# Performance work log

Measured on AMD Instinct MI355X. Metric: run time of the kernel, lower is better.

Reference implementation:

```python
import jax, jax.numpy as jnp
import numpy as np

def setup_inputs() -> dict:
    key = jax.random.key(0)
    k1, k2, k3 = jax.random.split(key, 3)
    B, NC, NQ, D = 16, 1024, 128, 512
    c_vector = jax.random.normal(k1, (B, NC, D), dtype=jnp.float32)
    q_vector = jax.random.normal(k2, (B, NQ, D), dtype=jnp.float32)
    kernel = jax.random.normal(k3, (3 * D, 1), dtype=jnp.float32) * 0.05
    bias = jnp.ones((), dtype=jnp.float32)
    return {"c_vector": c_vector, "q_vector": q_vector, "kernel": kernel, "bias": bias}

def reference(c_vector, q_vector, kernel, bias):
    # sim[b,i,j] = w . [c_i ; q_j ; c_i*q_j] + bias, decomposed to avoid the
    # (B, n_c, n_q, 3d) intermediate of the original tile+concat formulation.
    D = c_vector.shape[-1]
    w = kernel[:, 0]                      # (3d,)
    w_c, w_q, w_cq = w[:D], w[D:2 * D], w[2 * D:]
    c_term = c_vector @ w_c               # (B, n_c)
    q_term = q_vector @ w_q               # (B, n_q)
    cq_term = jnp.einsum('bid,bjd->bij', c_vector * w_cq, q_vector)  # (B, n_c, n_q)
    return cq_term + c_term[:, :, None] + q_term[:, None, :] + bias
```

## Files before the change

### kernel.cpp

```cpp
#include <hip/hip_runtime.h>
#include <hip/hip_bf16.h>

#define B_   16
#define NC_  1024
#define NQ_  128
#define D_   512
#define NKT  8

typedef __attribute__((ext_vector_type(8))) short bf16x8;
typedef __attribute__((ext_vector_type(4))) float f32x4;

__device__ __forceinline__ short f2bf(float x) {
    return __builtin_bit_cast(short, __float2bfloat16(x));
}
__device__ __forceinline__ float bf2f(short s) {
    unsigned u = ((unsigned)(unsigned short)s) << 16;
    return __builtin_bit_cast(float, u);
}

__global__ __launch_bounds__(256, 2) void sim_kernel(
    const float* __restrict__ c, const float* __restrict__ q,
    const float* __restrict__ kern, const float* __restrict__ bias_p,
    float* __restrict__ out)
{
    __shared__ __align__(16) char  lds[2][16384];
    __shared__ __align__(16) short wl[1536];
    __shared__ __align__(16) float ctl[64];
    __shared__ __align__(16) float qtl[64];

    const int bid   = blockIdx.x;
    const int b     = ((bid & 7) << 1) | (bid >> 8);
    const int inner = (bid >> 3) & 31;
    const int mt    = inner >> 1;
    const int nb    = inner & 1;
    const int tid   = threadIdx.x;
    const int lane  = tid & 63;
    const int w     = tid >> 6;
    const int wm    = w >> 1, wn = w & 1;
    const int rif   = lane & 15;
    const int kg    = lane >> 4;

    if (tid < 192) {
        const float* s = kern + tid * 8;
        f32x4 v0 = *(const f32x4*)s;
        f32x4 v1 = *(const f32x4*)(s + 4);
        bf16x8 o;
        o[0]=f2bf(v0[0]); o[1]=f2bf(v0[1]); o[2]=f2bf(v0[2]); o[3]=f2bf(v0[3]);
        o[4]=f2bf(v1[0]); o[5]=f2bf(v1[1]); o[6]=f2bf(v1[2]); o[7]=f2bf(v1[3]);
        *(bf16x8*)&wl[tid * 8] = o;
    }

    const int ar0 = tid >> 3, ar1 = ar0 + 32;
    const int acs = (tid & 7) * 8;
    const float* ag0 = c + (size_t)(b * NC_ + mt * 64 + ar0) * D_ + acs;
    const float* ag1 = c + (size_t)(b * NC_ + mt * 64 + ar1) * D_ + acs;
    const int aw0 = ar0 * 128 + ((acs * 2)       ^ ((ar0 & 7) << 4));
    const int aw1 = ar1 * 128 + ((acs * 2)       ^ ((ar1 & 7) << 4));

    const int bj = tid >> 2, bp = tid & 3;
    const float* bg = q + (size_t)(b * NQ_ + nb * 64 + bj) * D_ + bp * 16;
    const int bw0 = 8192 + bj * 128 + ((bp * 32)      ^ ((bj & 7) << 4));
    const int bw1 = 8192 + bj * 128 + ((bp * 32 + 16) ^ ((bj & 7) << 4));

    f32x4 sa[2][4], sb[2][4];
    float ct0 = 0.f, ct1 = 0.f, qta = 0.f;
    f32x4 acc00 = {}, acc01 = {}, acc10 = {}, acc11 = {};

#define ISSUE(T)                                                   \
    do { const int s_ = (T) & 1;                                   \
        sa[s_][0] = *(const f32x4*)(ag0 + (T) * 64);               \
        sa[s_][1] = *(const f32x4*)(ag0 + (T) * 64 + 4);           \
        sa[s_][2] = *(const f32x4*)(ag1 + (T) * 64);               \
        sa[s_][3] = *(const f32x4*)(ag1 + (T) * 64 + 4);           \
        sb[s_][0] = *(const f32x4*)(bg + (T) * 64);                \
        sb[s_][1] = *(const f32x4*)(bg + (T) * 64 + 4);            \
        sb[s_][2] = *(const f32x4*)(bg + (T) * 64 + 8);            \
        sb[s_][3] = *(const f32x4*)(bg + (T) * 64 + 12);           \
    } while (0)

#define WRITE(T)                                                               \
    do { const int s_ = (T) & 1; char* Lw = &lds[s_][0];                       \
        bf16x8 wcq = *(const bf16x8*)&wl[1024 + (T) * 64 + acs];               \
        bf16x8 wc8 = *(const bf16x8*)&wl[       (T) * 64 + acs];               \
        bf16x8 wq0 = *(const bf16x8*)&wl[512  + (T) * 64 + bp * 16];           \
        bf16x8 wq1 = *(const bf16x8*)&wl[512  + (T) * 64 + bp * 16 + 8];       \
        bf16x8 oa0, oa1, ob0, ob1;                                             \
        _Pragma("unroll")                                                      \
        for (int e = 0; e < 8; ++e) {                                          \
            float wcqf = bf2f(wcq[e]);                                         \
            float x0 = sa[s_][e >> 2][e & 3];                                  \
            float x1 = sa[s_][2 + (e >> 2)][e & 3];                            \
            oa0[e] = f2bf(x0 * wcqf);                                          \
            oa1[e] = f2bf(x1 * wcqf);                                          \
            float wcf = bf2f(wc8[e]);                                          \
            ct0 += x0 * wcf;  ct1 += x1 * wcf;                                 \
            float y0 = sb[s_][e >> 2][e & 3];                                  \
            float y1 = sb[s_][2 + (e >> 2)][e & 3];                            \
            ob0[e] = f2bf(y0); ob1[e] = f2bf(y1);                              \
            qta += y0 * bf2f(wq0[e]) + y1 * bf2f(wq1[e]);                      \
        }                                                                      \
        *(bf16x8*)(Lw + aw0) = oa0;                                            \
        *(bf16x8*)(Lw + aw1) = oa1;                                            \
        *(bf16x8*)(Lw + bw0) = ob0;                                            \
        *(bf16x8*)(Lw + bw1) = ob1;                                            \
    } while (0)

#define COMPUTE(T)                                                                                   \
    do { const char* L = &lds[(T) & 1][0];                                                           \
        _Pragma("unroll")                                                                            \
        for (int kk = 0; kk < 2; ++kk) {                                                             \
            const int ks = kk * 64 + kg * 16;                                                        \
            bf16x8 af0, af1, bf0, bf1;                                                               \
            { int r = wm*32 + rif;      af0 = *(const bf16x8*)(L + r*128 + (ks ^ ((r & 7) << 4))); } \
            { int r = wm*32 + 16 + rif; af1 = *(const bf16x8*)(L + r*128 + (ks ^ ((r & 7) << 4))); } \
            { int j = wn*32 + rif;      bf0 = *(const bf16x8*)(L + 8192 + j*128 + (ks ^ ((j & 7) << 4))); } \
            { int j = wn*32 + 16 + rif; bf1 = *(const bf16x8*)(L + 8192 + j*128 + (ks ^ ((j & 7) << 4))); } \
            acc00 = __builtin_amdgcn_mfma_f32_16x16x32_bf16(af0, bf0, acc00, 0, 0, 0);               \
            acc01 = __builtin_amdgcn_mfma_f32_16x16x32_bf16(af0, bf1, acc01, 0, 0, 0);               \
            acc10 = __builtin_amdgcn_mfma_f32_16x16x32_bf16(af1, bf0, acc10, 0, 0, 0);               \
            acc11 = __builtin_amdgcn_mfma_f32_16x16x32_bf16(af1, bf1, acc11, 0, 0, 0);               \
        }                                                                                            \
    } while (0)

    ISSUE(0); ISSUE(1);
    asm volatile("s_waitcnt lgkmcnt(0)" ::: "memory");
    __builtin_amdgcn_sched_barrier(0);
    __builtin_amdgcn_s_barrier();
    WRITE(0);
    asm volatile("s_waitcnt lgkmcnt(0)" ::: "memory");
    __builtin_amdgcn_sched_barrier(0);
    __builtin_amdgcn_s_barrier();

    #pragma unroll
    for (int kt = 0; kt < NKT; ++kt) {
        if (kt + 2 < NKT) ISSUE(kt + 2);
        __builtin_amdgcn_sched_barrier(0);
        COMPUTE(kt);
        if (kt + 1 < NKT) {
            WRITE(kt + 1);
            asm volatile("s_waitcnt lgkmcnt(0)" ::: "memory");
            __builtin_amdgcn_sched_barrier(0);
            __builtin_amdgcn_s_barrier();
        }
    }
#undef ISSUE
#undef WRITE
#undef COMPUTE

    ct0 += __shfl_xor(ct0, 1); ct0 += __shfl_xor(ct0, 2); ct0 += __shfl_xor(ct0, 4);
    ct1 += __shfl_xor(ct1, 1); ct1 += __shfl_xor(ct1, 2); ct1 += __shfl_xor(ct1, 4);
    qta += __shfl_xor(qta, 1); qta += __shfl_xor(qta, 2);
    if ((tid & 7) == 0) { ctl[ar0] = ct0; ctl[ar1] = ct1; }
    if ((tid & 3) == 0) qtl[bj] = qta;
    asm volatile("s_waitcnt lgkmcnt(0)" ::: "memory");
    __builtin_amdgcn_sched_barrier(0);
    __builtin_amdgcn_s_barrier();

    const float bias = *bias_p;
    const int jc = wn * 32;
    const float qt0 = qtl[jc + rif]      + bias;
    const float qt1 = qtl[jc + 16 + rif] + bias;
    #pragma unroll
    for (int mf = 0; mf < 2; ++mf) {
        f32x4 ctv = *(const f32x4*)&ctl[wm * 32 + mf * 16 + kg * 4];
        float* o = out + ((size_t)(b * NC_ + mt * 64 + wm * 32 + mf * 16 + kg * 4)) * NQ_
                 + nb * 64 + jc + rif;
        const f32x4 a0 = mf ? acc10 : acc00;
        const f32x4 a1 = mf ? acc11 : acc01;
        #pragma unroll
        for (int r = 0; r < 4; ++r) {
            o[(size_t)r * NQ_ +  0] = a0[r] + ctv[r] + qt0;
            o[(size_t)r * NQ_ + 16] = a1[r] + ctv[r] + qt1;
        }
    }
}

extern "C" void kernel_launch(void* const* d_in, const int* in_sizes, int n_in,
                              void* d_out, int out_size, void* d_ws, size_t ws_size,
                              hipStream_t stream) {
    const float* c    = (const float*)d_in[0];
    const float* q    = (const float*)d_in[1];
    const float* kern = (const float*)d_in[2];
    const float* bias = (const float*)d_in[3];
    float* out = (float*)d_out;

    sim_kernel<<<512, 256, 0, stream>>>(c, q, kern, bias, out);
}
```

Measured before the change: 16.36 us.

## Double the K-tile to 128, move w_cq scaling onto Q, cut pipeline depth

```diff
diff --git a/kernel.cpp b/kernel.cpp
--- a/kernel.cpp
+++ b/kernel.cpp
@@ -5,7 +5,7 @@
 #define NC_  1024
 #define NQ_  128
 #define D_   512
-#define NKT  8
+#define NKT  4
 
 typedef __attribute__((ext_vector_type(8))) short bf16x8;
 typedef __attribute__((ext_vector_type(4))) float f32x4;
@@ -23,8 +23,10 @@
     const float* __restrict__ kern, const float* __restrict__ bias_p,
     float* __restrict__ out)
 {
-    __shared__ __align__(16) char  lds[2][16384];
-    __shared__ __align__(16) short wl[1536];
+    __shared__ __align__(16) char  lds[2][32768];
+    __shared__ __align__(16) short wcb[512];
+    __shared__ __align__(16) short wqb[512];
+    __shared__ __align__(16) short wcqb[512];
     __shared__ __align__(16) float ctl[64];
     __shared__ __align__(16) float qtl[64];
 
@@ -47,74 +49,68 @@
         bf16x8 o;
         o[0]=f2bf(v0[0]); o[1]=f2bf(v0[1]); o[2]=f2bf(v0[2]); o[3]=f2bf(v0[3]);
         o[4]=f2bf(v1[0]); o[5]=f2bf(v1[1]); o[6]=f2bf(v1[2]); o[7]=f2bf(v1[3]);
-        *(bf16x8*)&wl[tid * 8] = o;
+        short* dst = (tid < 64) ? &wcb[tid * 8]
+                   : (tid < 128) ? &wqb[(tid - 64) * 8]
+                                 : &wcqb[(tid - 128) * 8];
+        *(bf16x8*)dst = o;
     }
 
-    const int ar0 = tid >> 3, ar1 = ar0 + 32;
-    const int acs = (tid & 7) * 8;
-    const float* ag0 = c + (size_t)(b * NC_ + mt * 64 + ar0) * D_ + acs;
-    const float* ag1 = c + (size_t)(b * NC_ + mt * 64 + ar1) * D_ + acs;
-    const int aw0 = ar0 * 128 + ((acs * 2)       ^ ((ar0 & 7) << 4));
-    const int aw1 = ar1 * 128 + ((acs * 2)       ^ ((ar1 & 7) << 4));
+    const int srow = tid >> 2;
+    const int scol = (tid & 3) * 32;
+    const float* ag = c + (size_t)(b * NC_ + mt * 64 + srow) * D_ + scol;
+    const float* bg = q + (size_t)(b * NQ_ + nb * 64 + srow) * D_ + scol;
+    int awc[4], bwc[4];
+    #pragma unroll
+    for (int i = 0; i < 4; ++i) {
+        const int off = ((tid & 3) * 64 + i * 16) ^ ((srow & 7) << 4);
+        awc[i] = srow * 256 + off;
+        bwc[i] = 16384 + srow * 256 + off;
+    }
 
-    const int bj = tid >> 2, bp = tid & 3;
-    const float* bg = q + (size_t)(b * NQ_ + nb * 64 + bj) * D_ + bp * 16;
-    const int bw0 = 8192 + bj * 128 + ((bp * 32)      ^ ((bj & 7) << 4));
-    const int bw1 = 8192 + bj * 128 + ((bp * 32 + 16) ^ ((bj & 7) << 4));
-
-    f32x4 sa[2][4], sb[2][4];
-    float ct0 = 0.f, ct1 = 0.f, qta = 0.f;
+    f32x4 sa[8], sb[8];
+    float cta = 0.f, qta = 0.f;
     f32x4 acc00 = {}, acc01 = {}, acc10 = {}, acc11 = {};
 
 #define ISSUE(T)                                                   \
-    do { const int s_ = (T) & 1;                                   \
-        sa[s_][0] = *(const f32x4*)(ag0 + (T) * 64);               \
-        sa[s_][1] = *(const f32x4*)(ag0 + (T) * 64 + 4);           \
-        sa[s_][2] = *(const f32x4*)(ag1 + (T) * 64);               \
-        sa[s_][3] = *(const f32x4*)(ag1 + (T) * 64 + 4);           \
-        sb[s_][0] = *(const f32x4*)(bg + (T) * 64);                \
-        sb[s_][1] = *(const f32x4*)(bg + (T) * 64 + 4);            \
-        sb[s_][2] = *(const f32x4*)(bg + (T) * 64 + 8);            \
-        sb[s_][3] = *(const f32x4*)(bg + (T) * 64 + 12);           \
+    do { _Pragma("unroll")                                         \
+        for (int i = 0; i < 8; ++i) {                              \
+            sa[i] = *(const f32x4*)(ag + (T) * 128 + i * 4);       \
+            sb[i] = *(const f32x4*)(bg + (T) * 128 + i * 4);       \
+        }                                                          \
     } while (0)
 
 #define WRITE(T)                                                               \
-    do { const int s_ = (T) & 1; char* Lw = &lds[s_][0];                       \
-        bf16x8 wcq = *(const bf16x8*)&wl[1024 + (T) * 64 + acs];               \
-        bf16x8 wc8 = *(const bf16x8*)&wl[       (T) * 64 + acs];               \
-        bf16x8 wq0 = *(const bf16x8*)&wl[512  + (T) * 64 + bp * 16];           \
-        bf16x8 wq1 = *(const bf16x8*)&wl[512  + (T) * 64 + bp * 16 + 8];       \
-        bf16x8 oa0, oa1, ob0, ob1;                                             \
+    do { char* Lw = &lds[(T) & 1][0];                                          \
         _Pragma("unroll")                                                      \
-        for (int e = 0; e < 8; ++e) {                                          \
-            float wcqf = bf2f(wcq[e]);                                         \
-            float x0 = sa[s_][e >> 2][e & 3];                                  \
-            float x1 = sa[s_][2 + (e >> 2)][e & 3];                            \
-            oa0[e] = f2bf(x0 * wcqf);                                          \
-            oa1[e] = f2bf(x1 * wcqf);                                          \
-            float wcf = bf2f(wc8[e]);                                          \
-            ct0 += x0 * wcf;  ct1 += x1 * wcf;                                 \
-            float y0 = sb[s_][e >> 2][e & 3];                                  \
-            float y1 = sb[s_][2 + (e >> 2)][e & 3];                            \
-            ob0[e] = f2bf(y0); ob1[e] = f2bf(y1);                              \
-            qta += y0 * bf2f(wq0[e]) + y1 * bf2f(wq1[e]);                      \
+        for (int g = 0; g < 4; ++g) {                                          \
+            bf16x8 wf  = *(const bf16x8*)&wcqb[(T) * 128 + scol + g * 8];      \
+            bf16x8 wc8 = *(const bf16x8*)&wcb [(T) * 128 + scol + g * 8];      \
+            bf16x8 wq8 = *(const bf16x8*)&wqb [(T) * 128 + scol + g * 8];      \
+            bf16x8 oa, ob;                                                     \
+            _Pragma("unroll")                                                  \
+            for (int e = 0; e < 8; ++e) {                                      \
+                float x = sa[g * 2 + (e >> 2)][e & 3];                         \
+                float y = sb[g * 2 + (e >> 2)][e & 3];                         \
+                oa[e] = f2bf(x);                                               \
+                ob[e] = f2bf(y * bf2f(wf[e]));                                 \
+                cta += x * bf2f(wc8[e]);                                       \
+                qta += y * bf2f(wq8[e]);                                       \
+            }                                                                  \
+            *(bf16x8*)(Lw + awc[g]) = oa;                                      \
+            *(bf16x8*)(Lw + bwc[g]) = ob;                                      \
         }                                                                      \
-        *(bf16x8*)(Lw + aw0) = oa0;                                            \
-        *(bf16x8*)(Lw + aw1) = oa1;                                            \
-        *(bf16x8*)(Lw + bw0) = ob0;                                            \
-        *(bf16x8*)(Lw + bw1) = ob1;                                            \
     } while (0)
 
 #define COMPUTE(T)                                                                                   \
     do { const char* L = &lds[(T) & 1][0];                                                           \
         _Pragma("unroll")                                                                            \
-        for (int kk = 0; kk < 2; ++kk) {                                                             \
-            const int ks = kk * 64 + kg * 16;                                                        \
+        for (int kk = 0; kk < 4; ++kk) {                                                             \
+            const int ksb = kk * 64 + kg * 16;                                                       \
             bf16x8 af0, af1, bf0, bf1;                                                               \
-            { int r = wm*32 + rif;      af0 = *(const bf16x8*)(L + r*128 + (ks ^ ((r & 7) << 4))); } \
-            { int r = wm*32 + 16 + rif; af1 = *(const bf16x8*)(L + r*128 + (ks ^ ((r & 7) << 4))); } \
-            { int j = wn*32 + rif;      bf0 = *(const bf16x8*)(L + 8192 + j*128 + (ks ^ ((j & 7) << 4))); } \
-            { int j = wn*32 + 16 + rif; bf1 = *(const bf16x8*)(L + 8192 + j*128 + (ks ^ ((j & 7) << 4))); } \
+            { int r = wm*32 + rif;      af0 = *(const bf16x8*)(L + r*256 + (ksb ^ ((r & 7) << 4))); } \
+            { int r = wm*32 + 16 + rif; af1 = *(const bf16x8*)(L + r*256 + (ksb ^ ((r & 7) << 4))); } \
+            { int j = wn*32 + rif;      bf0 = *(const bf16x8*)(L + 16384 + j*256 + (ksb ^ ((j & 7) << 4))); } \
+            { int j = wn*32 + 16 + rif; bf1 = *(const bf16x8*)(L + 16384 + j*256 + (ksb ^ ((j & 7) << 4))); } \
             acc00 = __builtin_amdgcn_mfma_f32_16x16x32_bf16(af0, bf0, acc00, 0, 0, 0);               \
             acc01 = __builtin_amdgcn_mfma_f32_16x16x32_bf16(af0, bf1, acc01, 0, 0, 0);               \
             acc10 = __builtin_amdgcn_mfma_f32_16x16x32_bf16(af1, bf0, acc10, 0, 0, 0);               \
@@ -122,7 +118,7 @@
         }                                                                                            \
     } while (0)
 
-    ISSUE(0); ISSUE(1);
+    ISSUE(0);
     asm volatile("s_waitcnt lgkmcnt(0)" ::: "memory");
     __builtin_amdgcn_sched_barrier(0);
     __builtin_amdgcn_s_barrier();
@@ -133,7 +129,7 @@
 
     #pragma unroll
     for (int kt = 0; kt < NKT; ++kt) {
-        if (kt + 2 < NKT) ISSUE(kt + 2);
+        if (kt + 1 < NKT) ISSUE(kt + 1);
         __builtin_amdgcn_sched_barrier(0);
         COMPUTE(kt);
         if (kt + 1 < NKT) {
@@ -147,30 +143,27 @@
 #undef WRITE
 #undef COMPUTE
 
-    ct0 += __shfl_xor(ct0, 1); ct0 += __shfl_xor(ct0, 2); ct0 += __shfl_xor(ct0, 4);
-    ct1 += __shfl_xor(ct1, 1); ct1 += __shfl_xor(ct1, 2); ct1 += __shfl_xor(ct1, 4);
+    cta += __shfl_xor(cta, 1); cta += __shfl_xor(cta, 2);
     qta += __shfl_xor(qta, 1); qta += __shfl_xor(qta, 2);
-    if ((tid & 7) == 0) { ctl[ar0] = ct0; ctl[ar1] = ct1; }
-    if ((tid & 3) == 0) qtl[bj] = qta;
+    if ((tid & 3) == 0) { ctl[srow] = cta; qtl[srow] = qta; }
     asm volatile("s_waitcnt lgkmcnt(0)" ::: "memory");
     __builtin_amdgcn_sched_barrier(0);
     __builtin_amdgcn_s_barrier();
 
     const float bias = *bias_p;
-    const int jc = wn * 32;
-    const float qt0 = qtl[jc + rif]      + bias;
-    const float qt1 = qtl[jc + 16 + rif] + bias;
+    const float q0 = qtl[wn * 32 + rif]      + bias;
+    const float q1 = qtl[wn * 32 + 16 + rif] + bias;
     #pragma unroll
     for (int mf = 0; mf < 2; ++mf) {
-        f32x4 ctv = *(const f32x4*)&ctl[wm * 32 + mf * 16 + kg * 4];
-        float* o = out + ((size_t)(b * NC_ + mt * 64 + wm * 32 + mf * 16 + kg * 4)) * NQ_
-                 + nb * 64 + jc + rif;
         const f32x4 a0 = mf ? acc10 : acc00;
         const f32x4 a1 = mf ? acc11 : acc01;
+        const f32x4 cv = *(const f32x4*)&ctl[wm * 32 + mf * 16 + kg * 4];
+        float* o = out + ((size_t)(b * NC_ + mt * 64 + wm * 32 + mf * 16 + kg * 4)) * NQ_
+                 + nb * 64 + wn * 32 + rif;
         #pragma unroll
         for (int r = 0; r < 4; ++r) {
-            o[(size_t)r * NQ_ +  0] = a0[r] + ctv[r] + qt0;
-            o[(size_t)r * NQ_ + 16] = a1[r] + ctv[r] + qt1;
+            o[(size_t)r * NQ_ +  0] = a0[r] + cv[r] + q0;
+            o[(size_t)r * NQ_ + 16] = a1[r] + cv[r] + q1;
         }
     }
 }
```

Measured after the change: 24.74 us. 1.51x slower.

## Halve M tile to 32 rows, launch 1024 blocks, move w_cq scaling onto Q

Applied to the files above, without the earlier changes.

```diff
diff --git a/kernel.cpp b/kernel.cpp
--- a/kernel.cpp
+++ b/kernel.cpp
@@ -18,19 +18,21 @@
     return __builtin_bit_cast(float, u);
 }
 
-__global__ __launch_bounds__(256, 2) void sim_kernel(
+__global__ __launch_bounds__(256, 4) void sim_kernel(
     const float* __restrict__ c, const float* __restrict__ q,
     const float* __restrict__ kern, const float* __restrict__ bias_p,
     float* __restrict__ out)
 {
-    __shared__ __align__(16) char  lds[2][16384];
-    __shared__ __align__(16) short wl[1536];
-    __shared__ __align__(16) float ctl[64];
+    __shared__ __align__(16) char  lds[2][12288];
+    __shared__ __align__(16) short wcb[512];
+    __shared__ __align__(16) short wqb[512];
+    __shared__ __align__(16) short wcqb[512];
+    __shared__ __align__(16) float ctl[32];
     __shared__ __align__(16) float qtl[64];
 
     const int bid   = blockIdx.x;
-    const int b     = ((bid & 7) << 1) | (bid >> 8);
-    const int inner = (bid >> 3) & 31;
+    const int b     = ((bid & 7) << 1) | (bid >> 9);
+    const int inner = (bid >> 3) & 63;
     const int mt    = inner >> 1;
     const int nb    = inner & 1;
     const int tid   = threadIdx.x;
@@ -47,31 +49,31 @@
         bf16x8 o;
         o[0]=f2bf(v0[0]); o[1]=f2bf(v0[1]); o[2]=f2bf(v0[2]); o[3]=f2bf(v0[3]);
         o[4]=f2bf(v1[0]); o[5]=f2bf(v1[1]); o[6]=f2bf(v1[2]); o[7]=f2bf(v1[3]);
-        *(bf16x8*)&wl[tid * 8] = o;
+        short* dst = (tid < 64) ? &wcb[tid * 8]
+                   : (tid < 128) ? &wqb[(tid - 64) * 8]
+                                 : &wcqb[(tid - 128) * 8];
+        *(bf16x8*)dst = o;
     }
 
-    const int ar0 = tid >> 3, ar1 = ar0 + 32;
+    const int ar  = tid >> 3;
     const int acs = (tid & 7) * 8;
-    const float* ag0 = c + (size_t)(b * NC_ + mt * 64 + ar0) * D_ + acs;
-    const float* ag1 = c + (size_t)(b * NC_ + mt * 64 + ar1) * D_ + acs;
-    const int aw0 = ar0 * 128 + ((acs * 2)       ^ ((ar0 & 7) << 4));
-    const int aw1 = ar1 * 128 + ((acs * 2)       ^ ((ar1 & 7) << 4));
+    const float* ag = c + (size_t)(b * NC_ + mt * 32 + ar) * D_ + acs;
+    const int awc = ar * 128 + ((acs * 2) ^ ((ar & 7) << 4));
 
-    const int bj = tid >> 2, bp = tid & 3;
-    const float* bg = q + (size_t)(b * NQ_ + nb * 64 + bj) * D_ + bp * 16;
-    const int bw0 = 8192 + bj * 128 + ((bp * 32)      ^ ((bj & 7) << 4));
-    const int bw1 = 8192 + bj * 128 + ((bp * 32 + 16) ^ ((bj & 7) << 4));
+    const int br  = tid >> 2;
+    const int bcs = (tid & 3) * 16;
+    const float* bg = q + (size_t)(b * NQ_ + nb * 64 + br) * D_ + bcs;
+    const int bwc0 = 4096 + br * 128 + ((bcs * 2)      ^ ((br & 7) << 4));
+    const int bwc1 = 4096 + br * 128 + ((bcs * 2 + 16) ^ ((br & 7) << 4));
 
-    f32x4 sa[2][4], sb[2][4];
-    float ct0 = 0.f, ct1 = 0.f, qta = 0.f;
-    f32x4 acc00 = {}, acc01 = {}, acc10 = {}, acc11 = {};
+    f32x4 sa[2][2], sb[2][4];
+    float cta = 0.f, qta = 0.f;
+    f32x4 acc0 = {}, acc1 = {};
 
 #define ISSUE(T)                                                   \
     do { const int s_ = (T) & 1;                                   \
-        sa[s_][0] = *(const f32x4*)(ag0 + (T) * 64);               \
-        sa[s_][1] = *(const f32x4*)(ag0 + (T) * 64 + 4);           \
-        sa[s_][2] = *(const f32x4*)(ag1 + (T) * 64);               \
-        sa[s_][3] = *(const f32x4*)(ag1 + (T) * 64 + 4);           \
+        sa[s_][0] = *(const f32x4*)(ag + (T) * 64);                \
+        sa[s_][1] = *(const f32x4*)(ag + (T) * 64 + 4);            \
         sb[s_][0] = *(const f32x4*)(bg + (T) * 64);                \
         sb[s_][1] = *(const f32x4*)(bg + (T) * 64 + 4);            \
         sb[s_][2] = *(const f32x4*)(bg + (T) * 64 + 8);            \
@@ -80,29 +82,30 @@
 
 #define WRITE(T)                                                               \
     do { const int s_ = (T) & 1; char* Lw = &lds[s_][0];                       \
-        bf16x8 wcq = *(const bf16x8*)&wl[1024 + (T) * 64 + acs];               \
-        bf16x8 wc8 = *(const bf16x8*)&wl[       (T) * 64 + acs];               \
-        bf16x8 wq0 = *(const bf16x8*)&wl[512  + (T) * 64 + bp * 16];           \
-        bf16x8 wq1 = *(const bf16x8*)&wl[512  + (T) * 64 + bp * 16 + 8];       \
-        bf16x8 oa0, oa1, ob0, ob1;                                             \
+        bf16x8 wc8 = *(const bf16x8*)&wcb [(T) * 64 + acs];                    \
+        bf16x8 oa;                                                             \
         _Pragma("unroll")                                                      \
         for (int e = 0; e < 8; ++e) {                                          \
-            float wcqf = bf2f(wcq[e]);                                         \
-            float x0 = sa[s_][e >> 2][e & 3];                                  \
-            float x1 = sa[s_][2 + (e >> 2)][e & 3];                            \
-            oa0[e] = f2bf(x0 * wcqf);                                          \
-            oa1[e] = f2bf(x1 * wcqf);                                          \
-            float wcf = bf2f(wc8[e]);                                          \
-            ct0 += x0 * wcf;  ct1 += x1 * wcf;                                 \
+            float x = sa[s_][e >> 2][e & 3];                                   \
+            oa[e] = f2bf(x);                                                   \
+            cta += x * bf2f(wc8[e]);                                           \
+        }                                                                      \
+        *(bf16x8*)(Lw + awc) = oa;                                             \
+        bf16x8 wf0 = *(const bf16x8*)&wcqb[(T) * 64 + bcs];                    \
+        bf16x8 wf1 = *(const bf16x8*)&wcqb[(T) * 64 + bcs + 8];                \
+        bf16x8 wq0 = *(const bf16x8*)&wqb [(T) * 64 + bcs];                    \
+        bf16x8 wq1 = *(const bf16x8*)&wqb [(T) * 64 + bcs + 8];                \
+        bf16x8 ob0, ob1;                                                       \
+        _Pragma("unroll")                                                      \
+        for (int e = 0; e < 8; ++e) {                                          \
             float y0 = sb[s_][e >> 2][e & 3];                                  \
             float y1 = sb[s_][2 + (e >> 2)][e & 3];                            \
-            ob0[e] = f2bf(y0); ob1[e] = f2bf(y1);                              \
+            ob0[e] = f2bf(y0 * bf2f(wf0[e]));                                  \
+            ob1[e] = f2bf(y1 * bf2f(wf1[e]));                                  \
             qta += y0 * bf2f(wq0[e]) + y1 * bf2f(wq1[e]);                      \
         }                                                                      \
-        *(bf16x8*)(Lw + aw0) = oa0;                                            \
-        *(bf16x8*)(Lw + aw1) = oa1;                                            \
-        *(bf16x8*)(Lw + bw0) = ob0;                                            \
-        *(bf16x8*)(Lw + bw1) = ob1;                                            \
+        *(bf16x8*)(Lw + bwc0) = ob0;                                           \
+        *(bf16x8*)(Lw + bwc1) = ob1;                                           \
     } while (0)
 
 #define COMPUTE(T)                                                                                   \
@@ -110,15 +113,12 @@
         _Pragma("unroll")                                                                            \
         for (int kk = 0; kk < 2; ++kk) {                                                             \
             const int ks = kk * 64 + kg * 16;                                                        \
-            bf16x8 af0, af1, bf0, bf1;                                                               \
-            { int r = wm*32 + rif;      af0 = *(const bf16x8*)(L + r*128 + (ks ^ ((r & 7) << 4))); } \
-            { int r = wm*32 + 16 + rif; af1 = *(const bf16x8*)(L + r*128 + (ks ^ ((r & 7) << 4))); } \
-            { int j = wn*32 + rif;      bf0 = *(const bf16x8*)(L + 8192 + j*128 + (ks ^ ((j & 7) << 4))); } \
-            { int j = wn*32 + 16 + rif; bf1 = *(const bf16x8*)(L + 8192 + j*128 + (ks ^ ((j & 7) << 4))); } \
-            acc00 = __builtin_amdgcn_mfma_f32_16x16x32_bf16(af0, bf0, acc00, 0, 0, 0);               \
-            acc01 = __builtin_amdgcn_mfma_f32_16x16x32_bf16(af0, bf1, acc01, 0, 0, 0);               \
-            acc10 = __builtin_amdgcn_mfma_f32_16x16x32_bf16(af1, bf0, acc10, 0, 0, 0);               \
-            acc11 = __builtin_amdgcn_mfma_f32_16x16x32_bf16(af1, bf1, acc11, 0, 0, 0);               \
+            bf16x8 af0, bf0, bf1;                                                                    \
+            { int r = wm*16 + rif;      af0 = *(const bf16x8*)(L + r*128 + (ks ^ ((r & 7) << 4))); } \
+            { int j = wn*32 + rif;      bf0 = *(const bf16x8*)(L + 4096 + j*128 + (ks ^ ((j & 7) << 4))); } \
+            { int j = wn*32 + 16 + rif; bf1 = *(const bf16x8*)(L + 4096 + j*128 + (ks ^ ((j & 7) << 4))); } \
+            acc0 = __builtin_amdgcn_mfma_f32_16x16x32_bf16(af0, bf0, acc0, 0, 0, 0);                 \
+            acc1 = __builtin_amdgcn_mfma_f32_16x16x32_bf16(af0, bf1, acc1, 0, 0, 0);                 \
         }                                                                                            \
     } while (0)
 
@@ -147,31 +147,24 @@
 #undef WRITE
 #undef COMPUTE
 
-    ct0 += __shfl_xor(ct0, 1); ct0 += __shfl_xor(ct0, 2); ct0 += __shfl_xor(ct0, 4);
-    ct1 += __shfl_xor(ct1, 1); ct1 += __shfl_xor(ct1, 2); ct1 += __shfl_xor(ct1, 4);
+    cta += __shfl_xor(cta, 1); cta += __shfl_xor(cta, 2); cta += __shfl_xor(cta, 4);
     qta += __shfl_xor(qta, 1); qta += __shfl_xor(qta, 2);
-    if ((tid & 7) == 0) { ctl[ar0] = ct0; ctl[ar1] = ct1; }
-    if ((tid & 3) == 0) qtl[bj] = qta;
+    if ((tid & 7) == 0) ctl[ar] = cta;
+    if ((tid & 3) == 0) qtl[br] = qta;
     asm volatile("s_waitcnt lgkmcnt(0)" ::: "memory");
     __builtin_amdgcn_sched_barrier(0);
     __builtin_amdgcn_s_barrier();
 
     const float bias = *bias_p;
-    const int jc = wn * 32;
-    const float qt0 = qtl[jc + rif]      + bias;
-    const float qt1 = qtl[jc + 16 + rif] + bias;
+    const float q0 = qtl[wn * 32 + rif]      + bias;
+    const float q1 = qtl[wn * 32 + 16 + rif] + bias;
+    const f32x4 cv = *(const f32x4*)&ctl[wm * 16 + kg * 4];
+    float* o = out + ((size_t)(b * NC_ + mt * 32 + wm * 16 + kg * 4)) * NQ_
+             + nb * 64 + wn * 32 + rif;
     #pragma unroll
-    for (int mf = 0; mf < 2; ++mf) {
-        f32x4 ctv = *(const f32x4*)&ctl[wm * 32 + mf * 16 + kg * 4];
-        float* o = out + ((size_t)(b * NC_ + mt * 64 + wm * 32 + mf * 16 + kg * 4)) * NQ_
-                 + nb * 64 + jc + rif;
-        const f32x4 a0 = mf ? acc10 : acc00;
-        const f32x4 a1 = mf ? acc11 : acc01;
-        #pragma unroll
-        for (int r = 0; r < 4; ++r) {
-            o[(size_t)r * NQ_ +  0] = a0[r] + ctv[r] + qt0;
-            o[(size_t)r * NQ_ + 16] = a1[r] + ctv[r] + qt1;
-        }
+    for (int r = 0; r < 4; ++r) {
+        o[(size_t)r * NQ_ +  0] = acc0[r] + cv[r] + q0;
+        o[(size_t)r * NQ_ + 16] = acc1[r] + cv[r] + q1;
     }
 }
 
@@ -184,5 +177,5 @@
     const float* bias = (const float*)d_in[3];
     float* out = (float*)d_out;
 
-    sim_kernel<<<512, 256, 0, stream>>>(c, q, kern, bias, out);
+    sim_kernel<<<1024, 256, 0, stream>>>(c, q, kern, bias, out);
 }
```

Result: slower. 19.14 us (+17.0%).
